# Optimization experiments

Hardware: AMD Instinct MI355X
Metric: run time of the kernel (lower is better)

Reference implementation:

```python
import jax, jax.numpy as jnp
import numpy as np

D_MODEL = 1024
NUM_HEADS = 16
HEAD_DIM = D_MODEL // NUM_HEADS
B, L = 4, 4096


def _linear(x, w, b):
    # torch nn.Linear: y = x @ w.T + b, w: [out, in]
    return jnp.einsum('bld,od->blo', x, w) + b


def _elu_feature_map(x):
    return jax.nn.elu(x) + 1.0


def setup_inputs() -> dict:
    key = jax.random.key(0)
    ks = jax.random.split(key, 11)
    s = 1.0 / np.sqrt(D_MODEL)
    inp = {
        'query': jax.random.normal(ks[0], (B, L, D_MODEL), jnp.float32),
        'key': jax.random.normal(ks[1], (B, L, D_MODEL), jnp.float32),
        'value': jax.random.normal(ks[2], (B, L, D_MODEL), jnp.float32),
        'wq': jax.random.uniform(ks[3], (D_MODEL, D_MODEL), jnp.float32, -s, s),
        'bq': jax.random.uniform(ks[4], (D_MODEL,), jnp.float32, -s, s),
        'wk': jax.random.uniform(ks[5], (D_MODEL, D_MODEL), jnp.float32, -s, s),
        'bk': jax.random.uniform(ks[6], (D_MODEL,), jnp.float32, -s, s),
        'wv': jax.random.uniform(ks[7], (D_MODEL, D_MODEL), jnp.float32, -s, s),
        'bv': jax.random.uniform(ks[8], (D_MODEL,), jnp.float32, -s, s),
        'wo': jax.random.uniform(ks[9], (D_MODEL, D_MODEL), jnp.float32, -s, s),
        'bo': jax.random.uniform(ks[10], (D_MODEL,), jnp.float32, -s, s),
    }
    return inp


def reference(query, key, value, wq, bq, wk, bk, wv, bv, wo, bo):
    Bsz, Lq, _ = query.shape
    # project and split heads -> [B, H, L, hd]
    def split_heads(x):
        return x.reshape(Bsz, -1, NUM_HEADS, HEAD_DIM).transpose(0, 2, 1, 3)
    Q = split_heads(_linear(query, wq, bq))
    K = split_heads(_linear(key, wk, bk))
    V = split_heads(_linear(value, wv, bv))
    Q = _elu_feature_map(Q)
    K = _elu_feature_map(K)
    # KV: [B, H, hd, hd]
    KV = jnp.einsum('bhld,bhle->bhde', K, V)
    Ksum = K.sum(axis=2)  # [B, H, hd]
    Z = 1.0 / (jnp.einsum('bhld,bhd->bhl', Q, Ksum) + 1e-6)  # [B, H, Lq]
    out = jnp.einsum('bhld,bhde->bhle', Q, KV) * Z[..., None]
    out = out.transpose(0, 2, 1, 3).reshape(Bsz, Lq, D_MODEL)
    return _linear(out, wo, bo)
```

## Files before the change

kernel.cpp:

```cpp
#include <hip/hip_runtime.h>
#include <hip/hip_bf16.h>

typedef _Float16 half8 __attribute__((ext_vector_type(8)));
typedef _Float16 half4 __attribute__((ext_vector_type(4)));
typedef float f32x4 __attribute__((ext_vector_type(4)));

#define KDIM 1024
#define NDIM 1024
#define MROWS 16384

#define GLD_LDS16(g, l)                                                  \
  __builtin_amdgcn_global_load_lds(                                      \
      (const __attribute__((address_space(1))) void*)(g),                \
      (__attribute__((address_space(3))) void*)(l), 16, 0, 0)

__global__ __launch_bounds__(256)
void cvt32(const float* __restrict__ s0, _Float16* __restrict__ d0,
           const float* __restrict__ s1, _Float16* __restrict__ d1,
           const float* __restrict__ s2, _Float16* __restrict__ d2,
           const float* __restrict__ s3, _Float16* __restrict__ d3) {
  const float* src;
  _Float16* dst;
  switch (blockIdx.y) {
    case 0: src = s0; dst = d0; break;
    case 1: src = s1; dst = d1; break;
    case 2: src = s2; dst = d2; break;
    default: src = s3; dst = d3; break;
  }
  const size_t g = (size_t)blockIdx.x * 8192;
  const int tid = threadIdx.x;
  float4 f[8];
#pragma unroll
  for (int j = 0; j < 8; ++j)
    f[j] = *(const float4*)(src + g + j * 1024 + tid * 4);
#pragma unroll
  for (int j = 0; j < 4; ++j) {
    half8 h;
    h[0] = (_Float16)f[2 * j].x;     h[1] = (_Float16)f[2 * j].y;
    h[2] = (_Float16)f[2 * j].z;     h[3] = (_Float16)f[2 * j].w;
    h[4] = (_Float16)f[2 * j + 1].x; h[5] = (_Float16)f[2 * j + 1].y;
    h[6] = (_Float16)f[2 * j + 1].z; h[7] = (_Float16)f[2 * j + 1].w;
    *(half4*)(dst + g + 2 * j * 1024 + tid * 4) = half4{h[0], h[1], h[2], h[3]};
    *(half4*)(dst + g + (2 * j + 1) * 1024 + tid * 4) = half4{h[4], h[5], h[6], h[7]};
  }
}

template <int ACT, int TRANS, int FUSE, typename TOUT>
__global__ __launch_bounds__(512, 2)
void gemm_bk32(const _Float16* __restrict__ X, const _Float16* __restrict__ W,
               const float* __restrict__ bias, TOUT* __restrict__ Y,
               const _Float16* __restrict__ KVTx) {
  constexpr int BM = 256, BN = 128, BK = 32;
  __shared__ char smem[73728];
  _Float16* As = (_Float16*)smem;
  _Float16* Bs = (_Float16*)(smem + 49152);

  const int tid  = threadIdx.x;
  const int lane = tid & 63;
  const int w    = tid >> 6;
  const int wm   = w >> 1;
  const int wn   = w & 1;

  const int bid = blockIdx.x;
  const int wid = (bid & 7) * 64 + (bid >> 3);
  const int m0  = (wid >> 3) * BM;
  const int n0  = (wid & 7) * BN;

  const int lrw = lane >> 2;
  const int gsl = (lane & 3) ^ (lrw & 3);
  const _Float16* gA = X + (size_t)(m0 + w * 16 + lrw) * KDIM + gsl * 8;
  const _Float16* gB = W + (size_t)(n0 + w * 16 + lrw) * KDIM + gsl * 8;

#define STAGE32(kt, bidx)                                                     \
  {                                                                           \
    const int k0s = (kt) * BK;                                                \
    _Float16* la = As + (bidx) * (BM * BK) + (w * 16) * BK;                   \
    _Float16* lb = Bs + (bidx) * (BN * BK) + (w * 16) * BK;                   \
    GLD_LDS16(gA + k0s, la);                                                  \
    GLD_LDS16(gA + (size_t)128 * KDIM + k0s, la + 128 * BK);                  \
    GLD_LDS16(gB + k0s, lb);                                                  \
  }

  const int rsl = ((lane >> 4) ^ (lane & 3)) << 4;

  f32x4 acc[4][4] = {};

  STAGE32(0, 0);
  STAGE32(1, 1);
  asm volatile("s_waitcnt vmcnt(3)" ::: "memory");
  asm volatile("s_barrier" ::: "memory");

  int bc = 0;
  for (int t = 0; t < 32; ++t) {
    int bs = bc + 2; if (bs >= 3) bs -= 3;
    const char* Ab = (const char*)As + bc * (BM * BK * 2);
    const char* Bb = (const char*)Bs + bc * (BN * BK * 2);

    half8 afr[4], bfr[4];
#pragma unroll
    for (int mi = 0; mi < 4; ++mi) {
      int row = wm * 64 + mi * 16 + (lane & 15);
      afr[mi] = *(const half8*)(Ab + row * 64 + rsl);
    }
#pragma unroll
    for (int ni = 0; ni < 4; ++ni) {
      int row = wn * 64 + ni * 16 + (lane & 15);
      bfr[ni] = *(const half8*)(Bb + row * 64 + rsl);
    }

    if (t < 30) STAGE32(t + 2, bs);

    __builtin_amdgcn_s_setprio(1);
#pragma unroll
    for (int mi = 0; mi < 4; ++mi)
#pragma unroll
      for (int ni = 0; ni < 4; ++ni)
        acc[mi][ni] = __builtin_amdgcn_mfma_f32_16x16x32_f16(
            afr[mi], bfr[ni], acc[mi][ni], 0, 0, 0);
    __builtin_amdgcn_s_setprio(0);

    if (t < 30) {
      asm volatile("s_waitcnt vmcnt(3)" ::: "memory");
      asm volatile("s_barrier" ::: "memory");
    } else if (t == 30) {
      asm volatile("s_waitcnt vmcnt(0)" ::: "memory");
      asm volatile("s_barrier" ::: "memory");
    }
    ++bc; if (bc == 3) bc = 0;
  }
#undef STAGE32

  if constexpr (FUSE) {
    __syncthreads();
    _Float16* Ct = (_Float16*)smem;
#pragma unroll
    for (int ni = 0; ni < 4; ++ni) {
      int cl   = wn * 64 + ni * 16 + (lane & 15);
      float bv = bias[n0 + cl];
#pragma unroll
      for (int mi = 0; mi < 4; ++mi) {
#pragma unroll
        for (int i = 0; i < 4; ++i) {
          int row = wm * 64 + mi * 16 + ((lane >> 4) << 2) + i;
          float v = acc[mi][ni][i] + bv;
          v = (v > 0.f) ? (v + 1.f) : __expf(v);
          int byte = row * 256 + cl * 2;
          byte ^= (row & 7) << 4;
          *(_Float16*)((char*)Ct + byte) = (_Float16)v;
        }
      }
    }
    __syncthreads();
    const int bh0 = ((m0 >> 12) << 4) + (n0 >> 6);
    const _Float16* kvp = KVTx + (size_t)(bh0 + wn) * 5120;
    f32x4 acc2[4][5] = {};
#pragma unroll
    for (int kk = 0; kk < 2; ++kk) {
      half8 afr2[4], bfr2[5];
#pragma unroll
      for (int m = 0; m < 4; ++m) {
        int row  = wm * 64 + m * 16 + (lane & 15);
        int byte = row * 256 + wn * 128 + kk * 64 + ((lane >> 4) << 4);
        byte ^= (row & 7) << 4;
        afr2[m] = *(const half8*)((const char*)Ct + byte);
      }
#pragma unroll
      for (int n = 0; n < 5; ++n) {
        int row = n * 16 + (lane & 15);
        bfr2[n] = *(const half8*)(kvp + row * 64 + kk * 32 + ((lane >> 4) << 3));
      }
#pragma unroll
      for (int m = 0; m < 4; ++m)
#pragma unroll
        for (int n = 0; n < 5; ++n)
          acc2[m][n] = __builtin_amdgcn_mfma_f32_16x16x32_f16(
              afr2[m], bfr2[n], acc2[m][n], 0, 0, 0);
    }
#pragma unroll
    for (int m = 0; m < 4; ++m) {
#pragma unroll
      for (int i = 0; i < 4; ++i) {
        float dn = __shfl(acc2[m][4][i], lane & 48);
        float z  = 1.f / (dn + 1e-6f);
        size_t row = (size_t)m0 + wm * 64 + m * 16 + ((lane >> 4) << 2) + i;
#pragma unroll
        for (int n = 0; n < 4; ++n) {
          int col = n0 + wn * 64 + n * 16 + (lane & 15);
          Y[row * NDIM + col] = (TOUT)(acc2[m][n][i] * z);
        }
      }
    }
    return;
  }

#pragma unroll
  for (int ni = 0; ni < 4; ++ni) {
    int col  = n0 + wn * 64 + ni * 16 + (lane & 15);
    float bv = bias[col];
#pragma unroll
    for (int mi = 0; mi < 4; ++mi) {
      int r0 = m0 + wm * 64 + mi * 16 + ((lane >> 4) << 2);
      if constexpr (TRANS) {
        int b  = r0 >> 12;
        int l0 = r0 & 4095;
        half4 hv;
#pragma unroll
        for (int i = 0; i < 4; ++i) {
          float v = acc[mi][ni][i] + bv;
          if constexpr (ACT == 1) v = (v > 0.f) ? (v + 1.f) : __expf(v);
          hv[i] = (_Float16)v;
        }
        *(half4*)((_Float16*)Y + ((size_t)(b * 1024 + col)) * 4096 + l0) = hv;
      } else {
#pragma unroll
        for (int i = 0; i < 4; ++i) {
          float v = acc[mi][ni][i] + bv;
          if constexpr (ACT == 1) v = (v > 0.f) ? (v + 1.f) : __expf(v);
          Y[(size_t)(r0 + i) * NDIM + col] = (TOUT)v;
        }
      }
    }
  }
}

__global__ __launch_bounds__(256, 2)
void kv_mfma(const _Float16* __restrict__ KT, const _Float16* __restrict__ VT,
             _Float16* __restrict__ pKV) {
  const int bh = blockIdx.x;
  const int ch = blockIdx.y;
  const int tid  = threadIdx.x;
  const int lane = tid & 63;
  const int w    = tid >> 6;

  __shared__ _Float16 As[64 * 64];
  __shared__ _Float16 Bs[64 * 64];

  const int lr = lane >> 3;
  const int ls = (lane & 7) ^ lr;
  const size_t lbase = (size_t)ch * 1024 + ls * 8;
  const _Float16* gA = VT + (size_t)(bh * 64 + w * 16 + lr) * 4096 + lbase;
  const _Float16* gB = KT + (size_t)(bh * 64 + w * 16 + lr) * 4096 + lbase;
  _Float16* ldsA = As + (w * 16) * 64;
  _Float16* ldsB = Bs + (w * 16) * 64;

  half8 aones;
#pragma unroll
  for (int j = 0; j < 8; ++j) aones[j] = (lane & 15) == 0 ? (_Float16)1.0f : (_Float16)0.0f;

  f32x4 acc[5] = {};

  for (int k0 = 0; k0 < 1024; k0 += 64) {
    __syncthreads();
#pragma unroll
    for (int c = 0; c < 2; ++c) {
      GLD_LDS16(gA + k0 + (size_t)(c * 8) * 4096, ldsA + c * 8 * 64);
      GLD_LDS16(gB + k0 + (size_t)(c * 8) * 4096, ldsB + c * 8 * 64);
    }
    __syncthreads();

    half8 afr[4][2], bfr[2];
#pragma unroll
    for (int m = 0; m < 4; ++m)
#pragma unroll
      for (int kk = 0; kk < 2; ++kk) {
        int row  = m * 16 + (lane & 15);
        int byte = row * 128 + ((lane >> 4) << 4) + kk * 64;
        byte ^= (row & 7) << 4;
        afr[m][kk] = *(const half8*)((const char*)As + byte);
      }
#pragma unroll
    for (int kk = 0; kk < 2; ++kk) {
      int row  = w * 16 + (lane & 15);
      int byte = row * 128 + ((lane >> 4) << 4) + kk * 64;
      byte ^= (row & 7) << 4;
      bfr[kk] = *(const half8*)((const char*)Bs + byte);
    }
#pragma unroll
    for (int kk = 0; kk < 2; ++kk) {
#pragma unroll
      for (int m = 0; m < 4; ++m)
        acc[m] = __builtin_amdgcn_mfma_f32_16x16x32_f16(afr[m][kk], bfr[kk],
                                                        acc[m], 0, 0, 0);
      acc[4] = __builtin_amdgcn_mfma_f32_16x16x32_f16(aones, bfr[kk],
                                                      acc[4], 0, 0, 0);
    }
  }

  _Float16* outp = pKV + ((size_t)ch * 64 + bh) * 5120;
  const int col = w * 16 + (lane & 15);
#pragma unroll
  for (int m = 0; m < 5; ++m) {
#pragma unroll
    for (int i = 0; i < 4; ++i) {
      int row = m * 16 + ((lane >> 4) << 2) + i;
      outp[row * 64 + col] = (_Float16)acc[m][i];
    }
  }
}

__global__ __launch_bounds__(256)
void kv_combine(const _Float16* __restrict__ pKV, _Float16* __restrict__ KVTx) {
  int g = blockIdx.x * 256 + threadIdx.x;
  int bh = g / 5120;
  int j  = g - bh * 5120;
  float s = 0.f;
#pragma unroll
  for (int ch = 0; ch < 4; ++ch)
    s += (float)pKV[((size_t)ch * 64 + bh) * 5120 + j];
  KVTx[(size_t)bh * 5120 + j] = (_Float16)s;
}

extern "C" void kernel_launch(void* const* d_in, const int* in_sizes, int n_in,
                              void* d_out, int out_size, void* d_ws, size_t ws_size,
                              hipStream_t stream) {
  const float* q  = (const float*)d_in[0];
  const float* k  = (const float*)d_in[1];
  const float* v  = (const float*)d_in[2];
  const float* wq = (const float*)d_in[3];
  const float* bq = (const float*)d_in[4];
  const float* wk = (const float*)d_in[5];
  const float* bk = (const float*)d_in[6];
  const float* wv = (const float*)d_in[7];
  const float* bv = (const float*)d_in[8];
  const float* wo = (const float*)d_in[9];
  const float* bo = (const float*)d_in[10];
  float* out = (float*)d_out;

  char* ws = (char*)d_ws;
  _Float16* Xq   = (_Float16*)(ws);
  _Float16* KT   = (_Float16*)(ws + 33554432);
  _Float16* VT   = (_Float16*)(ws + 67108864);
  _Float16* pKV  = (_Float16*)(ws + 100663296);
  _Float16* whk  = (_Float16*)(ws + 100663296);
  _Float16* whv  = (_Float16*)(ws + 102760448);
  _Float16* whq  = (_Float16*)(ws + 104857600);
  _Float16* who  = (_Float16*)(ws + 106954752);
  _Float16* att  = KT;
  _Float16* Xk   = (_Float16*)d_out;
  _Float16* Xv   = (_Float16*)((char*)d_out + 33554432);
  _Float16* KVTx = (_Float16*)((char*)d_out + 33554432);

  const int GBLK = (MROWS / 256) * (NDIM / 128);

  cvt32<<<dim3(128, 4), 256, 0, stream>>>(wq, whq, wk, whk, wv, whv, wo, who);
  cvt32<<<dim3(2048, 3), 256, 0, stream>>>(k, Xk, v, Xv, q, Xq, nullptr, nullptr);

  gemm_bk32<1, 1, 0, _Float16><<<GBLK, 512, 0, stream>>>(Xk, whk, bk, KT, nullptr);
  gemm_bk32<0, 1, 0, _Float16><<<GBLK, 512, 0, stream>>>(Xv, whv, bv, VT, nullptr);

  kv_mfma<<<dim3(64, 4), 256, 0, stream>>>(KT, VT, pKV);
  kv_combine<<<1280, 256, 0, stream>>>(pKV, KVTx);

  gemm_bk32<1, 0, 1, _Float16><<<GBLK, 512, 0, stream>>>(Xq, whq, bq, att, KVTx);

  gemm_bk32<0, 0, 0, float><<<GBLK, 512, 0, stream>>>(att, who, bo, out, nullptr);
}
```

Baseline: 258.1 us.

## Fuse fp32-to-fp16 input conversion into GEMM A-operand loads

Removes the separate conversion pass over the q/k/v activations. The projection GEMMs now read fp32 A tiles directly into registers, convert them to fp16 and write them swizzled into LDS, one stage ahead, while B still uses direct global-to-LDS loads. This avoids writing and re-reading 3x32MB of fp16 intermediates. In exchange the GEMM reads twice the A bytes, adds register pressure, and adds VALU conversion and LDS-store work inside the main loop. The workspace layout is reshuffled so that pKV/KVTx no longer live in the output buffer.

```diff
diff --git a/kernel.cpp b/kernel.cpp
--- a/kernel.cpp
+++ b/kernel.cpp
@@ -45,12 +45,13 @@
   }
 }
 
-template <int ACT, int TRANS, int FUSE, typename TOUT>
+template <int ACT, int TRANS, int FUSE, typename TA, typename TOUT>
 __global__ __launch_bounds__(512, 2)
-void gemm_bk32(const _Float16* __restrict__ X, const _Float16* __restrict__ W,
+void gemm_bk32(const TA* __restrict__ X, const _Float16* __restrict__ W,
                const float* __restrict__ bias, TOUT* __restrict__ Y,
                const _Float16* __restrict__ KVTx) {
   constexpr int BM = 256, BN = 128, BK = 32;
+  constexpr bool F32A = (sizeof(TA) == 4);
   __shared__ char smem[73728];
   _Float16* As = (_Float16*)smem;
   _Float16* Bs = (_Float16*)(smem + 49152);
@@ -68,30 +69,64 @@
 
   const int lrw = lane >> 2;
   const int gsl = (lane & 3) ^ (lrw & 3);
-  const _Float16* gA = X + (size_t)(m0 + w * 16 + lrw) * KDIM + gsl * 8;
   const _Float16* gB = W + (size_t)(n0 + w * 16 + lrw) * KDIM + gsl * 8;
-
-#define STAGE32(kt, bidx)                                                     \
+#define GLDB(kt, bidx)                                                        \
+  GLD_LDS16(gB + (kt) * BK, Bs + (bidx) * (BN * BK) + (w * 16) * BK)
+
+  const _Float16* gA16 =
+      (const _Float16*)X + (size_t)(m0 + w * 16 + lrw) * KDIM + gsl * 8;
+#define GLDA16(kt, bidx)                                                      \
   {                                                                           \
-    const int k0s = (kt) * BK;                                                \
     _Float16* la = As + (bidx) * (BM * BK) + (w * 16) * BK;                   \
-    _Float16* lb = Bs + (bidx) * (BN * BK) + (w * 16) * BK;                   \
-    GLD_LDS16(gA + k0s, la);                                                  \
-    GLD_LDS16(gA + (size_t)128 * KDIM + k0s, la + 128 * BK);                  \
-    GLD_LDS16(gB + k0s, lb);                                                  \
+    GLD_LDS16(gA16 + (kt) * BK, la);                                          \
+    GLD_LDS16(gA16 + (size_t)128 * KDIM + (kt) * BK, la + 128 * BK);          \
+  }
+  const int sr2 = tid >> 1;
+  const int kh  = tid & 1;
+  const float* gA32 = (const float*)X + (size_t)(m0 + sr2) * KDIM + kh * 16;
+  float4 ar[4];
+#define ISSUEA32(kt)                                                          \
+  {                                                                           \
+    _Pragma("unroll")                                                         \
+    for (int j = 0; j < 4; ++j)                                               \
+      ar[j] = *(const float4*)(gA32 + (kt) * BK + j * 4);                     \
+  }
+#define CVTWRA32(bidx)                                                        \
+  {                                                                           \
+    _Pragma("unroll")                                                         \
+    for (int j = 0; j < 2; ++j) {                                             \
+      half8 h;                                                                \
+      h[0] = (_Float16)ar[2 * j].x;     h[1] = (_Float16)ar[2 * j].y;         \
+      h[2] = (_Float16)ar[2 * j].z;     h[3] = (_Float16)ar[2 * j].w;         \
+      h[4] = (_Float16)ar[2 * j + 1].x; h[5] = (_Float16)ar[2 * j + 1].y;     \
+      h[6] = (_Float16)ar[2 * j + 1].z; h[7] = (_Float16)ar[2 * j + 1].w;     \
+      int slot = (kh * 2 + j) ^ (sr2 & 3);                                    \
+      *(half8*)((char*)As + (bidx) * 16384 + sr2 * 64 + slot * 16) = h;       \
+    }                                                                         \
   }
 
   const int rsl = ((lane >> 4) ^ (lane & 3)) << 4;
 
   f32x4 acc[4][4] = {};
 
-  STAGE32(0, 0);
-  STAGE32(1, 1);
-  asm volatile("s_waitcnt vmcnt(3)" ::: "memory");
-  asm volatile("s_barrier" ::: "memory");
+  if constexpr (F32A) {
+    ISSUEA32(0);
+    GLDB(0, 0);
+    GLDB(1, 1);
+    CVTWRA32(0);
+    ISSUEA32(1);
+    asm volatile("s_waitcnt vmcnt(5) lgkmcnt(0)" ::: "memory");
+    asm volatile("s_barrier" ::: "memory");
+  } else {
+    GLDA16(0, 0); GLDB(0, 0);
+    GLDA16(1, 1); GLDB(1, 1);
+    asm volatile("s_waitcnt vmcnt(3)" ::: "memory");
+    asm volatile("s_barrier" ::: "memory");
+  }
 
   int bc = 0;
   for (int t = 0; t < 32; ++t) {
+    int b1 = bc + 1; if (b1 == 3) b1 = 0;
     int bs = bc + 2; if (bs >= 3) bs -= 3;
     const char* Ab = (const char*)As + bc * (BM * BK * 2);
     const char* Bb = (const char*)Bs + bc * (BN * BK * 2);
@@ -108,7 +143,12 @@
       bfr[ni] = *(const half8*)(Bb + row * 64 + rsl);
     }
 
-    if (t < 30) STAGE32(t + 2, bs);
+    if constexpr (F32A) {
+      if (t < 31) CVTWRA32(b1);
+      if (t < 30) { ISSUEA32(t + 2); GLDB(t + 2, bs); }
+    } else {
+      if (t < 30) { GLDA16(t + 2, bs); GLDB(t + 2, bs); }
+    }
 
     __builtin_amdgcn_s_setprio(1);
 #pragma unroll
@@ -119,16 +159,29 @@
             afr[mi], bfr[ni], acc[mi][ni], 0, 0, 0);
     __builtin_amdgcn_s_setprio(0);
 
-    if (t < 30) {
-      asm volatile("s_waitcnt vmcnt(3)" ::: "memory");
-      asm volatile("s_barrier" ::: "memory");
-    } else if (t == 30) {
-      asm volatile("s_waitcnt vmcnt(0)" ::: "memory");
-      asm volatile("s_barrier" ::: "memory");
+    if constexpr (F32A) {
+      if (t < 30) {
+        asm volatile("s_waitcnt vmcnt(5) lgkmcnt(0)" ::: "memory");
+        asm volatile("s_barrier" ::: "memory");
+      } else if (t == 30) {
+        asm volatile("s_waitcnt vmcnt(0) lgkmcnt(0)" ::: "memory");
+        asm volatile("s_barrier" ::: "memory");
+      }
+    } else {
+      if (t < 30) {
+        asm volatile("s_waitcnt vmcnt(3)" ::: "memory");
+        asm volatile("s_barrier" ::: "memory");
+      } else if (t == 30) {
+        asm volatile("s_waitcnt vmcnt(0)" ::: "memory");
+        asm volatile("s_barrier" ::: "memory");
+      }
     }
     ++bc; if (bc == 3) bc = 0;
   }
-#undef STAGE32
+#undef GLDB
+#undef GLDA16
+#undef ISSUEA32
+#undef CVTWRA32
 
   if constexpr (FUSE) {
     __syncthreads();
@@ -327,31 +380,27 @@
   float* out = (float*)d_out;
 
   char* ws = (char*)d_ws;
-  _Float16* Xq   = (_Float16*)(ws);
+  _Float16* pKV  = (_Float16*)(ws);
+  _Float16* KVTx = (_Float16*)(ws + 4194304);
   _Float16* KT   = (_Float16*)(ws + 33554432);
   _Float16* VT   = (_Float16*)(ws + 67108864);
-  _Float16* pKV  = (_Float16*)(ws + 100663296);
   _Float16* whk  = (_Float16*)(ws + 100663296);
   _Float16* whv  = (_Float16*)(ws + 102760448);
   _Float16* whq  = (_Float16*)(ws + 104857600);
   _Float16* who  = (_Float16*)(ws + 106954752);
   _Float16* att  = KT;
-  _Float16* Xk   = (_Float16*)d_out;
-  _Float16* Xv   = (_Float16*)((char*)d_out + 33554432);
-  _Float16* KVTx = (_Float16*)((char*)d_out + 33554432);
 
   const int GBLK = (MROWS / 256) * (NDIM / 128);
 
   cvt32<<<dim3(128, 4), 256, 0, stream>>>(wq, whq, wk, whk, wv, whv, wo, who);
-  cvt32<<<dim3(2048, 3), 256, 0, stream>>>(k, Xk, v, Xv, q, Xq, nullptr, nullptr);
-
-  gemm_bk32<1, 1, 0, _Float16><<<GBLK, 512, 0, stream>>>(Xk, whk, bk, KT, nullptr);
-  gemm_bk32<0, 1, 0, _Float16><<<GBLK, 512, 0, stream>>>(Xv, whv, bv, VT, nullptr);
+
+  gemm_bk32<1, 1, 0, float, _Float16><<<GBLK, 512, 0, stream>>>(k, whk, bk, KT, nullptr);
+  gemm_bk32<0, 1, 0, float, _Float16><<<GBLK, 512, 0, stream>>>(v, whv, bv, VT, nullptr);
 
   kv_mfma<<<dim3(64, 4), 256, 0, stream>>>(KT, VT, pKV);
   kv_combine<<<1280, 256, 0, stream>>>(pKV, KVTx);
 
-  gemm_bk32<1, 0, 1, _Float16><<<GBLK, 512, 0, stream>>>(Xq, whq, bq, att, KVTx);
-
-  gemm_bk32<0, 0, 0, float><<<GBLK, 512, 0, stream>>>(att, who, bo, out, nullptr);
+  gemm_bk32<1, 0, 1, float, _Float16><<<GBLK, 512, 0, stream>>>(q, whq, bq, att, KVTx);
+
+  gemm_bk32<0, 0, 0, _Float16, float><<<GBLK, 512, 0, stream>>>(att, who, bo, out, nullptr);
 }
```

Result: slower. 296.3 us (+14.8%).
